# Kernel optimization log

Hardware: AMD Instinct MI355X
Metric: run time of the kernel (lower is better)

## Reference

```python
import jax, jax.numpy as jnp
import numpy as np

HIDDEN = 1024
FFN = 4096
NUM_EXPERTS = 8
TOP_K = 2
LOAD_BALANCE_WEIGHT = 0.01


def setup_inputs() -> dict:
    key = jax.random.key(0)
    ks = jax.random.split(key, 6)
    B, S = 4, 2048
    x = jax.random.normal(ks[0], (B, S, HIDDEN), dtype=jnp.float32)
    router_w = jax.random.normal(ks[1], (NUM_EXPERTS, HIDDEN), dtype=jnp.float32) * 0.02
    fc1_w = jax.random.normal(ks[2], (NUM_EXPERTS, FFN, HIDDEN), dtype=jnp.float32) * 0.02
    fc1_b = jnp.zeros((NUM_EXPERTS, FFN), dtype=jnp.float32)
    fc2_w = jax.random.normal(ks[3], (NUM_EXPERTS, HIDDEN, FFN), dtype=jnp.float32) * 0.02
    fc2_b = jnp.zeros((NUM_EXPERTS, HIDDEN), dtype=jnp.float32)
    return {"x": x, "router_w": router_w, "fc1_w": fc1_w, "fc1_b": fc1_b,
            "fc2_w": fc2_w, "fc2_b": fc2_b}


def reference(x, router_w, fc1_w, fc1_b, fc2_w, fc2_b):
    B, S, H = x.shape
    xf = x.reshape(-1, H)                       # [T, H]
    T = xf.shape[0]
    logits = xf @ router_w.T                    # [T, E]
    probs = jax.nn.softmax(logits, axis=-1)
    weights, indices = jax.lax.top_k(probs, TOP_K)   # [T, K]
    weights = weights / jnp.sum(weights, axis=-1, keepdims=True)
    # combine weight per (token, expert): sum of top-k weights assigned to expert
    onehot = jax.nn.one_hot(indices, NUM_EXPERTS, dtype=xf.dtype)  # [T, K, E]
    combine = jnp.sum(weights[..., None] * onehot, axis=1)          # [T, E]
    out = jnp.zeros_like(xf)
    for e in range(NUM_EXPERTS):
        h = jax.nn.gelu(xf @ fc1_w[e].T + fc1_b[e], approximate=False)
        y = h @ fc2_w[e].T + fc2_b[e]
        # tokens not routed to expert e have combine weight 0 -> contribute 0,
        # matching the torch masked gather/scatter-add exactly (dropout in eval).
        out = out + y * combine[:, e:e + 1]
    # load-balance aux loss
    counts = jnp.sum(onehot, axis=(0, 1))                # bincount of indices
    freq = counts / (T * TOP_K)
    aux_loss = LOAD_BALANCE_WEIGHT * NUM_EXPERTS * jnp.sum(jnp.mean(probs, axis=0) * freq)
    return out.reshape(B, S, H), aux_loss
```

## Files before the change

### kernel.cpp

```cpp
#include <hip/hip_runtime.h>
#include <math.h>

#define T_TOK 8192
#define HID 1024
#define FFN_DIM 4096
#define NEXP 8
#define BM 128
#define MAX_TILES 136

typedef __attribute__((ext_vector_type(8))) __bf16 bf16x8;
typedef __attribute__((ext_vector_type(8))) unsigned short ushort8;
typedef __attribute__((ext_vector_type(4))) float f32x4;

static __device__ __forceinline__ unsigned short f2bf(float f) {
  unsigned u = __builtin_bit_cast(unsigned, f);
  u += 0x7FFFu + ((u >> 16) & 1u);
  return (unsigned short)(u >> 16);
}

static __device__ __forceinline__ void gl16(const void* g, void* l) {
  __builtin_amdgcn_global_load_lds((const __attribute__((address_space(1))) unsigned int*)g,
                                   (__attribute__((address_space(3))) unsigned int*)l,
                                   16, 0, 0);
}

static __device__ __forceinline__ ushort8 cvt8(const float* p) {
  float4 a = *(const float4*)p, b = *(const float4*)(p + 4);
  ushort8 o;
  o[0] = f2bf(a.x); o[1] = f2bf(a.y); o[2] = f2bf(a.z); o[3] = f2bf(a.w);
  o[4] = f2bf(b.x); o[5] = f2bf(b.y); o[6] = f2bf(b.z); o[7] = f2bf(b.w);
  return o;
}

__global__ void moe_cvt_w(const float* __restrict__ w1, const float* __restrict__ w2,
                          unsigned short* __restrict__ w1b, unsigned short* __restrict__ w2b) {
  size_t i = ((size_t)blockIdx.x * 256 + threadIdx.x) * 8;
  if (blockIdx.y == 0) *(ushort8*)(w1b + i) = cvt8(w1 + i);
  else                 *(ushort8*)(w2b + i) = cvt8(w2 + i);
}

__global__ void moe_router(const float* __restrict__ x, const float* __restrict__ rw,
                           int* __restrict__ tok_idx, float* __restrict__ tok_w,
                           float* __restrict__ pbuf, unsigned short* __restrict__ xb) {
  int t = blockIdx.x * 4 + (threadIdx.x >> 6);
  int lane = threadIdx.x & 63;
  const float* xr = x + (size_t)t * HID;
  unsigned short* xbr = xb + (size_t)t * HID;
  double acc[NEXP];
#pragma unroll
  for (int e = 0; e < NEXP; ++e) acc[e] = 0.0;
  for (int i = 0; i < HID / 64; ++i) {
    float xv = xr[lane + 64 * i];
    xbr[lane + 64 * i] = f2bf(xv);
#pragma unroll
    for (int e = 0; e < NEXP; ++e)
      acc[e] += (double)xv * (double)rw[e * HID + lane + 64 * i];
  }
#pragma unroll
  for (int off = 32; off; off >>= 1)
#pragma unroll
    for (int e = 0; e < NEXP; ++e) acc[e] += __shfl_xor(acc[e], off);
  if (lane == 0) {
    double m = acc[0];
#pragma unroll
    for (int e = 1; e < NEXP; ++e) m = acc[e] > m ? acc[e] : m;
    float pf[NEXP], s = 0.0f;
#pragma unroll
    for (int e = 0; e < NEXP; ++e) { pf[e] = expf((float)(acc[e] - m)); s += pf[e]; }
    int i0 = 0;
#pragma unroll
    for (int e = 1; e < NEXP; ++e) if (acc[e] > acc[i0]) i0 = e;
    int i1 = (i0 == 0) ? 1 : 0;
#pragma unroll
    for (int e = 0; e < NEXP; ++e) if (e != i0 && acc[e] > acc[i1]) i1 = e;
    float w0 = pf[i0], w1 = pf[i1], wsum = w0 + w1;
    tok_idx[2 * t] = i0; tok_idx[2 * t + 1] = i1;
    tok_w[2 * t] = w0 / wsum; tok_w[2 * t + 1] = w1 / wsum;
    float inv = 1.0f / s;
#pragma unroll
    for (int e = 0; e < NEXP; ++e) pbuf[(size_t)t * NEXP + e] = pf[e] * inv;
  }
}

__global__ void moe_scatter(const int* __restrict__ tok_idx,
                            int* __restrict__ cursor, int* __restrict__ list,
                            int* __restrict__ inv) {
  const int e = blockIdx.x;
  __shared__ int wsum[16];
  __shared__ int base;
  const int tid = threadIdx.x, lane = tid & 63, wv = tid >> 6;
  if (tid == 0) base = 0;
  __syncthreads();
  for (int c = 0; c < 2 * T_TOK; c += 1024) {
    int i = c + tid;
    int m = (tok_idx[i] == e) ? 1 : 0;
    unsigned long long bal = __ballot(m);
    if (lane == 0) wsum[wv] = __popcll(bal);
    __syncthreads();
    int wbase = base;
    for (int k = 0; k < wv; ++k) wbase += wsum[k];
    if (m) {
      int pos = wbase + __popcll(bal & ((1ull << lane) - 1ull));
      list[e * T_TOK + pos] = i >> 1;
      inv[i] = (e << 13) | pos;
    }
    __syncthreads();
    if (tid == 0) {
      int s = 0;
#pragma unroll
      for (int k = 0; k < 16; ++k) s += wsum[k];
      base += s;
    }
    __syncthreads();
  }
  if (tid == 0) cursor[e] = base;
}

__global__ void moe_preduce(const float* __restrict__ pbuf, float* __restrict__ probs_sum) {
  const int e = blockIdx.x;
  float s = 0.0f;
  for (int t = threadIdx.x; t < T_TOK; t += 256) s += pbuf[(size_t)t * NEXP + e];
  __shared__ float red[4];
#pragma unroll
  for (int off = 32; off; off >>= 1) s += __shfl_down(s, off);
  if ((threadIdx.x & 63) == 0) red[threadIdx.x >> 6] = s;
  __syncthreads();
  if (threadIdx.x == 0) probs_sum[e] = red[0] + red[1] + red[2] + red[3];
}

__global__ void moe_offsets(const int* __restrict__ cursor, int* __restrict__ offs,
                            int* __restrict__ tile_e, int* __restrict__ tile_m,
                            int* __restrict__ meta) {
  if (threadIdx.x == 0 && blockIdx.x == 0) {
    int o = 0, t = 0;
    for (int e = 0; e < NEXP; ++e) {
      offs[e] = o;
      int ntl = (cursor[e] + BM - 1) / BM;
      for (int k = 0; k < ntl; ++k) { tile_e[t] = e; tile_m[t] = k; ++t; }
      o += ntl * BM;
    }
    offs[NEXP] = o;
    meta[0] = t;
  }
}

__global__ __launch_bounds__(256, 4) void moe_fc1(
    const unsigned short* __restrict__ xb, const unsigned short* __restrict__ w1b,
    const float* __restrict__ b1, const int* __restrict__ list,
    const int* __restrict__ offs, const int* __restrict__ tile_e,
    const int* __restrict__ tile_m, const int* __restrict__ meta,
    unsigned short* __restrict__ hbuf, int cb, int ch) {
  const int bid = blockIdx.x;
  const int c = bid & 7;
  const int k = bid >> 3;
  const int tl = c * 17 + k % 17;
  const int nt = k / 17;
  if (tl >= meta[0]) return;
  const int e = tile_e[tl], mt = tile_m[tl];
  __shared__ __align__(16) char As[BM * 128];
  __shared__ __align__(16) char Bs[BM * 128];
  const int tid = threadIdx.x, lane = tid & 63, wv = tid >> 6;
  const int wr = wv >> 1, wc = wv & 1;
  const int swz = ((lane & 7) ^ (lane >> 3)) << 4;
  const int rsub = lane >> 3;
  const int* le = list + e * T_TOK + mt * BM;
  const char* asrc[4]; const char* bsrc[4];
  char* adst[4]; char* bdst[4];
#pragma unroll
  for (int j = 0; j < 4; ++j) {
    int r = wv * 32 + j * 8 + rsub;
    int tok = le[r]; tok = tok < 0 ? 0 : tok;
    asrc[j] = (const char*)(xb + (size_t)tok * HID) + swz;
    bsrc[j] = (const char*)(w1b + ((size_t)e * FFN_DIM + cb + nt * BM + r) * HID) + swz;
    adst[j] = As + (wv * 32 + j * 8) * 128;
    bdst[j] = Bs + (wv * 32 + j * 8) * 128;
  }
  f32x4 acc[4][4] = {};
  for (int kt = 0; kt < 16; ++kt) {
    if (kt) __syncthreads();
#pragma unroll
    for (int j = 0; j < 4; ++j) {
      gl16(asrc[j] + kt * 128, adst[j]);
      gl16(bsrc[j] + kt * 128, bdst[j]);
    }
    __syncthreads();
#pragma unroll
    for (int kh = 0; kh < 2; ++kh) {
      bf16x8 afr[4], bfr[4];
      const int kb = kh * 64 + ((lane >> 4) << 4);
#pragma unroll
      for (int m = 0; m < 4; ++m) {
        int row = wr * 64 + m * 16 + (lane & 15);
        afr[m] = *(const bf16x8*)(As + row * 128 + (kb ^ ((row & 7) << 4)));
      }
#pragma unroll
      for (int n = 0; n < 4; ++n) {
        int col = wc * 64 + n * 16 + (lane & 15);
        bfr[n] = *(const bf16x8*)(Bs + col * 128 + (kb ^ ((col & 7) << 4)));
      }
#pragma unroll
      for (int m = 0; m < 4; ++m)
#pragma unroll
        for (int n = 0; n < 4; ++n)
          acc[m][n] = __builtin_amdgcn_mfma_f32_16x16x32_bf16(afr[m], bfr[n], acc[m][n], 0, 0, 0);
    }
  }
  const float* b1e = b1 + (size_t)e * FFN_DIM + cb + nt * BM;
  const size_t rbase = (size_t)(offs[e] + mt * BM);
#pragma unroll
  for (int n = 0; n < 4; ++n) {
    int cl = wc * 64 + n * 16 + (lane & 15);
    float bias = b1e[cl];
#pragma unroll
    for (int m = 0; m < 4; ++m)
#pragma unroll
      for (int j = 0; j < 4; ++j) {
        int rl = wr * 64 + m * 16 + ((lane >> 4) << 2) + j;
        float v = acc[m][n][j] + bias;
        float g = 0.5f * v * (1.0f + erff(v * 0.70710678118654752f));
        hbuf[(rbase + rl) * ch + nt * BM + cl] = f2bf(g);
      }
  }
}

__global__ __launch_bounds__(256, 4) void moe_fc2(
    const unsigned short* __restrict__ hbuf, const unsigned short* __restrict__ w2b,
    const float* __restrict__ b2, const int* __restrict__ offs,
    const int* __restrict__ tile_e, const int* __restrict__ tile_m,
    const int* __restrict__ meta, float* __restrict__ ybuf, int cb, int ch) {
  const int bid = blockIdx.x;
  const int c = bid & 7;
  const int k = bid >> 3;
  const int tl = c * 17 + (k >> 3);
  const int nt = k & 7;
  if (tl >= meta[0]) return;
  const int e = tile_e[tl], mt = tile_m[tl];
  __shared__ __align__(16) char As[BM * 128];
  __shared__ __align__(16) char Bs[BM * 128];
  const int tid = threadIdx.x, lane = tid & 63, wv = tid >> 6;
  const int wr = wv >> 1, wc = wv & 1;
  const int swz = ((lane & 7) ^ (lane >> 3)) << 4;
  const int rsub = lane >> 3;
  const size_t rbase = (size_t)(offs[e] + mt * BM);
  const char* asrc[4]; const char* bsrc[4];
  char* adst[4]; char* bdst[4];
#pragma unroll
  for (int j = 0; j < 4; ++j) {
    int r = wv * 32 + j * 8 + rsub;
    asrc[j] = (const char*)(hbuf + (rbase + r) * ch) + swz;
    bsrc[j] = (const char*)(w2b + ((size_t)e * HID + nt * BM + r) * FFN_DIM + cb) + swz;
    adst[j] = As + (wv * 32 + j * 8) * 128;
    bdst[j] = Bs + (wv * 32 + j * 8) * 128;
  }
  f32x4 acc[4][4] = {};
  const int nK = ch / 64;
  for (int kt = 0; kt < nK; ++kt) {
    if (kt) __syncthreads();
#pragma unroll
    for (int j = 0; j < 4; ++j) {
      gl16(asrc[j] + kt * 128, adst[j]);
      gl16(bsrc[j] + kt * 128, bdst[j]);
    }
    __syncthreads();
#pragma unroll
    for (int kh = 0; kh < 2; ++kh) {
      bf16x8 afr[4], bfr[4];
      const int kb = kh * 64 + ((lane >> 4) << 4);
#pragma unroll
      for (int m = 0; m < 4; ++m) {
        int row = wr * 64 + m * 16 + (lane & 15);
        afr[m] = *(const bf16x8*)(As + row * 128 + (kb ^ ((row & 7) << 4)));
      }
#pragma unroll
      for (int n = 0; n < 4; ++n) {
        int col = wc * 64 + n * 16 + (lane & 15);
        bfr[n] = *(const bf16x8*)(Bs + col * 128 + (kb ^ ((col & 7) << 4)));
      }
#pragma unroll
      for (int m = 0; m < 4; ++m)
#pragma unroll
        for (int n = 0; n < 4; ++n)
          acc[m][n] = __builtin_amdgcn_mfma_f32_16x16x32_bf16(afr[m], bfr[n], acc[m][n], 0, 0, 0);
    }
  }
  const float* b2e = b2 + (size_t)e * HID + nt * BM;
#pragma unroll
  for (int m = 0; m < 4; ++m)
#pragma unroll
    for (int j = 0; j < 4; ++j) {
      int rl = wr * 64 + m * 16 + ((lane >> 4) << 2) + j;
      float* yrow = ybuf + (rbase + rl) * HID + nt * BM;
#pragma unroll
      for (int n = 0; n < 4; ++n) {
        int cl = wc * 64 + n * 16 + (lane & 15);
        float v = acc[m][n][j];
        if (cb == 0) yrow[cl] = v + b2e[cl];
        else         yrow[cl] += v;
      }
    }
}

__global__ void moe_combine(const float* __restrict__ ybuf, const int* __restrict__ inv,
                            const float* __restrict__ tok_w, const int* __restrict__ offs,
                            float* __restrict__ out) {
  const int t = blockIdx.x;
  const int col = threadIdx.x * 4;
  int v0 = inv[2 * t], v1 = inv[2 * t + 1];
  size_t r0 = (size_t)(offs[v0 >> 13] + (v0 & 8191));
  size_t r1 = (size_t)(offs[v1 >> 13] + (v1 & 8191));
  float w0 = tok_w[2 * t], w1 = tok_w[2 * t + 1];
  float4 a = *(const float4*)(ybuf + r0 * HID + col);
  float4 b = *(const float4*)(ybuf + r1 * HID + col);
  float4 o;
  o.x = w0 * a.x + w1 * b.x;
  o.y = w0 * a.y + w1 * b.y;
  o.z = w0 * a.z + w1 * b.z;
  o.w = w0 * a.w + w1 * b.w;
  *(float4*)(out + (size_t)t * HID + col) = o;
}

__global__ void moe_finalize(const float* __restrict__ probs_sum, const int* __restrict__ cursor,
                             float* __restrict__ out_aux) {
  if (threadIdx.x == 0 && blockIdx.x == 0) {
    float a = 0.0f;
    for (int e = 0; e < NEXP; ++e)
      a += (probs_sum[e] / (float)T_TOK) * ((float)cursor[e] / (float)(T_TOK * 2));
    out_aux[0] = 0.01f * (float)NEXP * a;
  }
}

extern "C" void kernel_launch(void* const* d_in, const int* in_sizes, int n_in,
                              void* d_out, int out_size, void* d_ws, size_t ws_size,
                              hipStream_t stream) {
  const float* x  = (const float*)d_in[0];
  const float* rw = (const float*)d_in[1];
  const float* w1 = (const float*)d_in[2];
  const float* b1 = (const float*)d_in[3];
  const float* w2 = (const float*)d_in[4];
  const float* b2 = (const float*)d_in[5];
  float* out = (float*)d_out;

  char* ws = (char*)d_ws;
  float* probs_sum = (float*)(ws + 0);
  int*   cursor    = (int*)(ws + 256);
  int*   meta      = (int*)(ws + 512);
  int*   offs      = (int*)(ws + 1024);
  int*   tile_e    = (int*)(ws + 2048);
  int*   tile_m    = (int*)(ws + 4096);
  int*   tok_idx   = (int*)(ws + 8192);
  float* tok_w     = (float*)(ws + 8192 + 65536);
  int*   list      = (int*)(ws + 8192 + 131072);
  float* pbuf      = (float*)(ws + 8192 + 655360);
  int*   inv       = (int*)(ws + 925696);
  unsigned short* xb   = (unsigned short*)(ws + 1048576);
  unsigned short* w1be = (unsigned short*)(ws + 17825792);
  unsigned short* w2be = (unsigned short*)(ws + 84934656);
  float* ybuf = (float*)(ws + 152043520);
  const size_t HBUF_OFF = 223346688;
  unsigned short* hbuf = (unsigned short*)(ws + HBUF_OFF);

  int CH = 4096;
  while (CH > 1024 && HBUF_OFF + (size_t)(MAX_TILES * BM) * CH * 2 > ws_size) CH >>= 1;

  hipMemsetAsync(ws + 8192 + 131072, 0xFF, 262144, stream);

  moe_cvt_w<<<dim3(16384, 2), 256, 0, stream>>>(w1, w2, w1be, w2be);
  moe_router<<<T_TOK / 4, 256, 0, stream>>>(x, rw, tok_idx, tok_w, pbuf, xb);
  moe_scatter<<<NEXP, 1024, 0, stream>>>(tok_idx, cursor, list, inv);
  moe_preduce<<<NEXP, 256, 0, stream>>>(pbuf, probs_sum);
  moe_offsets<<<1, 1, 0, stream>>>(cursor, offs, tile_e, tile_m, meta);

  for (int cb = 0; cb < FFN_DIM; cb += CH) {
    moe_fc1<<<MAX_TILES * (CH / BM), 256, 0, stream>>>(
        xb, w1be, b1, list, offs, tile_e, tile_m, meta, hbuf, cb, CH);
    moe_fc2<<<MAX_TILES * 8, 256, 0, stream>>>(
        hbuf, w2be, b2, offs, tile_e, tile_m, meta, ybuf, cb, CH);
  }
  moe_combine<<<T_TOK, 256, 0, stream>>>(ybuf, inv, tok_w, offs, out);
  moe_finalize<<<1, 64, 0, stream>>>(probs_sum, cursor, out + (size_t)T_TOK * HID);
}
```

Before: 607.6 us.

## Switch grouped expert GEMMs to 256x256 tiles with double-buffered LDS

Replaces the 128x128 tile, 256-thread fc1/fc2 kernels with 256x256 tiles computed by 512 threads, each wave holding a 128x64 accumulator block. Global-to-LDS loads are double-buffered across 128KB of shared memory, so the next K slice is fetched while MFMAs run and one barrier per K step is saved. The larger tiles double operand reuse per byte loaded, but each expert's row count is now padded to a multiple of 256 instead of 128, which adds wasted rows, and occupancy drops to one block per CU with fewer blocks per launch. Tile metadata and workspace offsets are resized to match.

```diff
diff --git a/kernel.cpp b/kernel.cpp
--- a/kernel.cpp
+++ b/kernel.cpp
@@ -5,8 +5,7 @@
 #define HID 1024
 #define FFN_DIM 4096
 #define NEXP 8
-#define BM 128
-#define MAX_TILES 136
+#define ROWS_CAP 18432
 
 typedef __attribute__((ext_vector_type(8))) __bf16 bf16x8;
 typedef __attribute__((ext_vector_type(8))) unsigned short ushort8;
@@ -129,171 +128,172 @@
 }
 
 __global__ void moe_offsets(const int* __restrict__ cursor, int* __restrict__ offs,
-                            int* __restrict__ tile_e, int* __restrict__ tile_m,
+                            int* __restrict__ te2, int* __restrict__ tm2,
                             int* __restrict__ meta) {
   if (threadIdx.x == 0 && blockIdx.x == 0) {
-    int o = 0, t = 0;
+    int o = 0, t2 = 0;
     for (int e = 0; e < NEXP; ++e) {
       offs[e] = o;
-      int ntl = (cursor[e] + BM - 1) / BM;
-      for (int k = 0; k < ntl; ++k) { tile_e[t] = e; tile_m[t] = k; ++t; }
-      o += ntl * BM;
+      int n2 = (cursor[e] + 255) >> 8;
+      for (int k = 0; k < n2; ++k) { te2[t2] = e; tm2[t2] = k; ++t2; }
+      o += n2 << 8;
     }
     offs[NEXP] = o;
-    meta[0] = t;
-  }
-}
-
-__global__ __launch_bounds__(256, 4) void moe_fc1(
+    meta[1] = t2;
+  }
+}
+
+#define ST_A(buf, k, h) do { char* d_ = L + (buf) + ((h) << 14) + (wv << 10); \
+    gl16(aptr[h][0] + (size_t)(k) * 128, d_); \
+    gl16(aptr[h][1] + (size_t)(k) * 128, d_ + 8192); } while (0)
+#define ST_B(buf, k, h) do { char* d_ = L + (buf) + 32768 + ((h) << 14) + (wv << 10); \
+    gl16(bptr[h][0] + (size_t)(k) * 128, d_); \
+    gl16(bptr[h][1] + (size_t)(k) * 128, d_ + 8192); } while (0)
+
+#define GEMM_CORE(NKVAL)                                                        \
+  f32x4 acc[8][4] = {};                                                         \
+  const int nK = (NKVAL);                                                       \
+  ST_A(0, 0, 0); ST_A(0, 0, 1); ST_B(0, 0, 0); ST_B(0, 0, 1);                   \
+  __syncthreads();                                                              \
+  for (int kt = 0; kt < nK; ++kt) {                                             \
+    const int pofs = (kt & 1) << 16;                                            \
+    if (kt + 1 < nK) {                                                          \
+      const int nofs = pofs ^ 65536;                                            \
+      ST_A(nofs, kt + 1, 0); ST_A(nofs, kt + 1, 1);                             \
+      ST_B(nofs, kt + 1, 0); ST_B(nofs, kt + 1, 1);                             \
+    }                                                                           \
+    _Pragma("unroll")                                                           \
+    for (int q = 0; q < 4; ++q) {                                               \
+      const int mh = q >> 1, nh = q & 1;                                        \
+      bf16x8 afr[4][2], bfr[2][2];                                              \
+      _Pragma("unroll")                                                         \
+      for (int i = 0; i < 4; ++i) {                                             \
+        const int ra = ((mh * 4 + i) * 16 + l15) << 7;                          \
+        _Pragma("unroll")                                                       \
+        for (int kk = 0; kk < 2; ++kk)                                          \
+          afr[i][kk] = *(const bf16x8*)(Abase + pofs + ra + (((kk << 6) + hi16) ^ rsw)); \
+      }                                                                         \
+      _Pragma("unroll")                                                         \
+      for (int jn = 0; jn < 2; ++jn) {                                          \
+        const int rb = ((nh * 2 + jn) * 16 + l15) << 7;                         \
+        _Pragma("unroll")                                                       \
+        for (int kk = 0; kk < 2; ++kk)                                          \
+          bfr[jn][kk] = *(const bf16x8*)(Bbase + pofs + rb + (((kk << 6) + hi16) ^ rsw)); \
+      }                                                                         \
+      _Pragma("unroll")                                                         \
+      for (int i = 0; i < 4; ++i)                                               \
+        _Pragma("unroll")                                                       \
+        for (int jn = 0; jn < 2; ++jn)                                          \
+          _Pragma("unroll")                                                     \
+          for (int kk = 0; kk < 2; ++kk)                                        \
+            acc[mh * 4 + i][nh * 2 + jn] = __builtin_amdgcn_mfma_f32_16x16x32_bf16( \
+                afr[i][kk], bfr[jn][kk], acc[mh * 4 + i][nh * 2 + jn], 0, 0, 0); \
+    }                                                                           \
+    __syncthreads();                                                            \
+  }
+
+__global__ __launch_bounds__(512, 1) void moe_fc1(
     const unsigned short* __restrict__ xb, const unsigned short* __restrict__ w1b,
     const float* __restrict__ b1, const int* __restrict__ list,
-    const int* __restrict__ offs, const int* __restrict__ tile_e,
-    const int* __restrict__ tile_m, const int* __restrict__ meta,
+    const int* __restrict__ offs, const int* __restrict__ te2,
+    const int* __restrict__ tm2, const int* __restrict__ meta,
     unsigned short* __restrict__ hbuf, int cb, int ch) {
-  const int bid = blockIdx.x;
-  const int c = bid & 7;
-  const int k = bid >> 3;
-  const int tl = c * 17 + k % 17;
-  const int nt = k / 17;
-  if (tl >= meta[0]) return;
-  const int e = tile_e[tl], mt = tile_m[tl];
-  __shared__ __align__(16) char As[BM * 128];
-  __shared__ __align__(16) char Bs[BM * 128];
+  const int ntc2 = ch >> 8;
+  const int c = blockIdx.x & 7;
+  const int q0 = blockIdx.x >> 3;
+  const int tl = c * 9 + q0 / ntc2;
+  const int nt = q0 % ntc2;
+  if (tl >= meta[1]) return;
+  const int e = te2[tl], mt = tm2[tl];
+  __shared__ __align__(16) char L[131072];
   const int tid = threadIdx.x, lane = tid & 63, wv = tid >> 6;
-  const int wr = wv >> 1, wc = wv & 1;
-  const int swz = ((lane & 7) ^ (lane >> 3)) << 4;
-  const int rsub = lane >> 3;
-  const int* le = list + e * T_TOK + mt * BM;
-  const char* asrc[4]; const char* bsrc[4];
-  char* adst[4]; char* bdst[4];
-#pragma unroll
-  for (int j = 0; j < 4; ++j) {
-    int r = wv * 32 + j * 8 + rsub;
-    int tok = le[r]; tok = tok < 0 ? 0 : tok;
-    asrc[j] = (const char*)(xb + (size_t)tok * HID) + swz;
-    bsrc[j] = (const char*)(w1b + ((size_t)e * FFN_DIM + cb + nt * BM + r) * HID) + swz;
-    adst[j] = As + (wv * 32 + j * 8) * 128;
-    bdst[j] = Bs + (wv * 32 + j * 8) * 128;
-  }
-  f32x4 acc[4][4] = {};
-  for (int kt = 0; kt < 16; ++kt) {
-    if (kt) __syncthreads();
+  const int wm = wv >> 2, wn = wv & 3;
+  const int l15 = lane & 15, hi16 = lane & 48;
+  const int rsw = (lane & 7) << 4;
+  const int chunk = ((lane & 7) ^ ((lane >> 3) & 7)) << 4;
+  const int rr = lane >> 3;
+  const char* Abase = L + (wm << 14);
+  const char* Bbase = L + 32768 + (wn << 13);
+
+  const int* le = list + e * T_TOK + mt * 256;
+  const char* aptr[2][2]; const char* bptr[2][2];
+#pragma unroll
+  for (int h = 0; h < 2; ++h)
+#pragma unroll
+    for (int c64 = 0; c64 < 2; ++c64) {
+      int r = h * 128 + c64 * 64 + wv * 8 + rr;
+      int tok = le[r]; tok = tok < 0 ? 0 : tok;
+      aptr[h][c64] = (const char*)(xb + (size_t)tok * HID) + chunk;
+      bptr[h][c64] = (const char*)(w1b + ((size_t)e * FFN_DIM + cb + nt * 256 + r) * HID) + chunk;
+    }
+
+  GEMM_CORE(HID / 64)
+
+  const float* b1e = b1 + (size_t)e * FFN_DIM + cb + nt * 256 + (wn << 6);
+  const size_t rbase = (size_t)(offs[e] + mt * 256);
+  float bias[4];
+#pragma unroll
+  for (int nf = 0; nf < 4; ++nf) bias[nf] = b1e[nf * 16 + l15];
+#pragma unroll
+  for (int m = 0; m < 8; ++m)
 #pragma unroll
     for (int j = 0; j < 4; ++j) {
-      gl16(asrc[j] + kt * 128, adst[j]);
-      gl16(bsrc[j] + kt * 128, bdst[j]);
-    }
-    __syncthreads();
-#pragma unroll
-    for (int kh = 0; kh < 2; ++kh) {
-      bf16x8 afr[4], bfr[4];
-      const int kb = kh * 64 + ((lane >> 4) << 4);
-#pragma unroll
-      for (int m = 0; m < 4; ++m) {
-        int row = wr * 64 + m * 16 + (lane & 15);
-        afr[m] = *(const bf16x8*)(As + row * 128 + (kb ^ ((row & 7) << 4)));
+      int row = (wm << 7) + m * 16 + ((lane >> 4) << 2) + j;
+      unsigned short* hrow = hbuf + (rbase + row) * ch + nt * 256 + (wn << 6);
+#pragma unroll
+      for (int nf = 0; nf < 4; ++nf) {
+        float v = acc[m][nf][j] + bias[nf];
+        float g = 0.5f * v * (1.0f + erff(v * 0.70710678118654752f));
+        hrow[nf * 16 + l15] = f2bf(g);
       }
-#pragma unroll
-      for (int n = 0; n < 4; ++n) {
-        int col = wc * 64 + n * 16 + (lane & 15);
-        bfr[n] = *(const bf16x8*)(Bs + col * 128 + (kb ^ ((col & 7) << 4)));
-      }
-#pragma unroll
-      for (int m = 0; m < 4; ++m)
-#pragma unroll
-        for (int n = 0; n < 4; ++n)
-          acc[m][n] = __builtin_amdgcn_mfma_f32_16x16x32_bf16(afr[m], bfr[n], acc[m][n], 0, 0, 0);
-    }
-  }
-  const float* b1e = b1 + (size_t)e * FFN_DIM + cb + nt * BM;
-  const size_t rbase = (size_t)(offs[e] + mt * BM);
-#pragma unroll
-  for (int n = 0; n < 4; ++n) {
-    int cl = wc * 64 + n * 16 + (lane & 15);
-    float bias = b1e[cl];
-#pragma unroll
-    for (int m = 0; m < 4; ++m)
-#pragma unroll
-      for (int j = 0; j < 4; ++j) {
-        int rl = wr * 64 + m * 16 + ((lane >> 4) << 2) + j;
-        float v = acc[m][n][j] + bias;
-        float g = 0.5f * v * (1.0f + erff(v * 0.70710678118654752f));
-        hbuf[(rbase + rl) * ch + nt * BM + cl] = f2bf(g);
-      }
-  }
-}
-
-__global__ __launch_bounds__(256, 4) void moe_fc2(
+    }
+}
+
+__global__ __launch_bounds__(512, 1) void moe_fc2(
     const unsigned short* __restrict__ hbuf, const unsigned short* __restrict__ w2b,
     const float* __restrict__ b2, const int* __restrict__ offs,
-    const int* __restrict__ tile_e, const int* __restrict__ tile_m,
+    const int* __restrict__ te2, const int* __restrict__ tm2,
     const int* __restrict__ meta, float* __restrict__ ybuf, int cb, int ch) {
-  const int bid = blockIdx.x;
-  const int c = bid & 7;
-  const int k = bid >> 3;
-  const int tl = c * 17 + (k >> 3);
-  const int nt = k & 7;
-  if (tl >= meta[0]) return;
-  const int e = tile_e[tl], mt = tile_m[tl];
-  __shared__ __align__(16) char As[BM * 128];
-  __shared__ __align__(16) char Bs[BM * 128];
+  const int c = blockIdx.x & 7;
+  const int q0 = blockIdx.x >> 3;
+  const int tl = c * 9 + (q0 >> 2);
+  const int nt = q0 & 3;
+  if (tl >= meta[1]) return;
+  const int e = te2[tl], mt = tm2[tl];
+  __shared__ __align__(16) char L[131072];
   const int tid = threadIdx.x, lane = tid & 63, wv = tid >> 6;
-  const int wr = wv >> 1, wc = wv & 1;
-  const int swz = ((lane & 7) ^ (lane >> 3)) << 4;
-  const int rsub = lane >> 3;
-  const size_t rbase = (size_t)(offs[e] + mt * BM);
-  const char* asrc[4]; const char* bsrc[4];
-  char* adst[4]; char* bdst[4];
-#pragma unroll
-  for (int j = 0; j < 4; ++j) {
-    int r = wv * 32 + j * 8 + rsub;
-    asrc[j] = (const char*)(hbuf + (rbase + r) * ch) + swz;
-    bsrc[j] = (const char*)(w2b + ((size_t)e * HID + nt * BM + r) * FFN_DIM + cb) + swz;
-    adst[j] = As + (wv * 32 + j * 8) * 128;
-    bdst[j] = Bs + (wv * 32 + j * 8) * 128;
-  }
-  f32x4 acc[4][4] = {};
-  const int nK = ch / 64;
-  for (int kt = 0; kt < nK; ++kt) {
-    if (kt) __syncthreads();
+  const int wm = wv >> 2, wn = wv & 3;
+  const int l15 = lane & 15, hi16 = lane & 48;
+  const int rsw = (lane & 7) << 4;
+  const int chunk = ((lane & 7) ^ ((lane >> 3) & 7)) << 4;
+  const int rr = lane >> 3;
+  const char* Abase = L + (wm << 14);
+  const char* Bbase = L + 32768 + (wn << 13);
+
+  const size_t rbase = (size_t)(offs[e] + mt * 256);
+  const char* aptr[2][2]; const char* bptr[2][2];
+#pragma unroll
+  for (int h = 0; h < 2; ++h)
+#pragma unroll
+    for (int c64 = 0; c64 < 2; ++c64) {
+      int r = h * 128 + c64 * 64 + wv * 8 + rr;
+      aptr[h][c64] = (const char*)(hbuf + (rbase + r) * ch) + chunk;
+      bptr[h][c64] = (const char*)(w2b + ((size_t)e * HID + nt * 256 + r) * FFN_DIM + cb) + chunk;
+    }
+
+  GEMM_CORE(ch / 64)
+
+  const float* b2e = b2 + (size_t)e * HID + nt * 256 + (wn << 6);
+#pragma unroll
+  for (int m = 0; m < 8; ++m)
 #pragma unroll
     for (int j = 0; j < 4; ++j) {
-      gl16(asrc[j] + kt * 128, adst[j]);
-      gl16(bsrc[j] + kt * 128, bdst[j]);
-    }
-    __syncthreads();
-#pragma unroll
-    for (int kh = 0; kh < 2; ++kh) {
-      bf16x8 afr[4], bfr[4];
-      const int kb = kh * 64 + ((lane >> 4) << 4);
-#pragma unroll
-      for (int m = 0; m < 4; ++m) {
-        int row = wr * 64 + m * 16 + (lane & 15);
-        afr[m] = *(const bf16x8*)(As + row * 128 + (kb ^ ((row & 7) << 4)));
-      }
-#pragma unroll
-      for (int n = 0; n < 4; ++n) {
-        int col = wc * 64 + n * 16 + (lane & 15);
-        bfr[n] = *(const bf16x8*)(Bs + col * 128 + (kb ^ ((col & 7) << 4)));
-      }
-#pragma unroll
-      for (int m = 0; m < 4; ++m)
-#pragma unroll
-        for (int n = 0; n < 4; ++n)
-          acc[m][n] = __builtin_amdgcn_mfma_f32_16x16x32_bf16(afr[m], bfr[n], acc[m][n], 0, 0, 0);
-    }
-  }
-  const float* b2e = b2 + (size_t)e * HID + nt * BM;
-#pragma unroll
-  for (int m = 0; m < 4; ++m)
-#pragma unroll
-    for (int j = 0; j < 4; ++j) {
-      int rl = wr * 64 + m * 16 + ((lane >> 4) << 2) + j;
-      float* yrow = ybuf + (rbase + rl) * HID + nt * BM;
-#pragma unroll
-      for (int n = 0; n < 4; ++n) {
-        int cl = wc * 64 + n * 16 + (lane & 15);
-        float v = acc[m][n][j];
+      int row = (wm << 7) + m * 16 + ((lane >> 4) << 2) + j;
+      float* yrow = ybuf + (rbase + row) * HID + nt * 256 + (wn << 6);
+#pragma unroll
+      for (int nf = 0; nf < 4; ++nf) {
+        int cl = nf * 16 + l15;
+        float v = acc[m][nf][j];
         if (cb == 0) yrow[cl] = v + b2e[cl];
         else         yrow[cl] += v;
       }
@@ -345,8 +345,8 @@
   int*   cursor    = (int*)(ws + 256);
   int*   meta      = (int*)(ws + 512);
   int*   offs      = (int*)(ws + 1024);
-  int*   tile_e    = (int*)(ws + 2048);
-  int*   tile_m    = (int*)(ws + 4096);
+  int*   tile_e2   = (int*)(ws + 5120);
+  int*   tile_m2   = (int*)(ws + 6144);
   int*   tok_idx   = (int*)(ws + 8192);
   float* tok_w     = (float*)(ws + 8192 + 65536);
   int*   list      = (int*)(ws + 8192 + 131072);
@@ -356,11 +356,11 @@
   unsigned short* w1be = (unsigned short*)(ws + 17825792);
   unsigned short* w2be = (unsigned short*)(ws + 84934656);
   float* ybuf = (float*)(ws + 152043520);
-  const size_t HBUF_OFF = 223346688;
+  const size_t HBUF_OFF = 227540992;
   unsigned short* hbuf = (unsigned short*)(ws + HBUF_OFF);
 
   int CH = 4096;
-  while (CH > 1024 && HBUF_OFF + (size_t)(MAX_TILES * BM) * CH * 2 > ws_size) CH >>= 1;
+  while (CH > 1024 && HBUF_OFF + (size_t)ROWS_CAP * CH * 2 > ws_size) CH >>= 1;
 
   hipMemsetAsync(ws + 8192 + 131072, 0xFF, 262144, stream);
 
@@ -368,13 +368,13 @@
   moe_router<<<T_TOK / 4, 256, 0, stream>>>(x, rw, tok_idx, tok_w, pbuf, xb);
   moe_scatter<<<NEXP, 1024, 0, stream>>>(tok_idx, cursor, list, inv);
   moe_preduce<<<NEXP, 256, 0, stream>>>(pbuf, probs_sum);
-  moe_offsets<<<1, 1, 0, stream>>>(cursor, offs, tile_e, tile_m, meta);
+  moe_offsets<<<1, 1, 0, stream>>>(cursor, offs, tile_e2, tile_m2, meta);
 
   for (int cb = 0; cb < FFN_DIM; cb += CH) {
-    moe_fc1<<<MAX_TILES * (CH / BM), 256, 0, stream>>>(
-        xb, w1be, b1, list, offs, tile_e, tile_m, meta, hbuf, cb, CH);
-    moe_fc2<<<MAX_TILES * 8, 256, 0, stream>>>(
-        hbuf, w2be, b2, offs, tile_e, tile_m, meta, ybuf, cb, CH);
+    moe_fc1<<<8 * 9 * (CH / 256), 512, 0, stream>>>(
+        xb, w1be, b1, list, offs, tile_e2, tile_m2, meta, hbuf, cb, CH);
+    moe_fc2<<<8 * 9 * 4, 512, 0, stream>>>(
+        hbuf, w2be, b2, offs, tile_e2, tile_m2, meta, ybuf, cb, CH);
   }
   moe_combine<<<T_TOK, 256, 0, stream>>>(ybuf, inv, tok_w, offs, out);
   moe_finalize<<<1, 64, 0, stream>>>(probs_sum, cursor, out + (size_t)T_TOK * HID);
```

New measurement: 636.4 us. 1.05x slower.
